# Optimization experiments

Measured on AMD Instinct MI355X. Metric: run time of the kernel, lower is better.

The kernel has to match this reference:

```python
import jax, jax.numpy as jnp
import numpy as np

B, T, D, K = 8, 4096, 512, 4096


def setup_inputs() -> dict:
    key = jax.random.key(0)
    k1, k2 = jax.random.split(key)
    x = jax.random.normal(k1, (B, T, D), dtype=jnp.float32)
    embed = jax.random.normal(k2, (K, D), dtype=jnp.float32)
    return {"x": x, "embed": embed}


def reference(x, embed):
    # F.normalize(x, p=2, dim=-1) with eps clamp like torch (eps=1e-12)
    norm = jnp.sqrt(jnp.sum(x * x, axis=-1, keepdims=True))
    xn = x / jnp.maximum(norm, 1e-12)

    flat = xn.reshape(-1, D)  # [(B*T), D]
    x_sq = jnp.sum(flat * flat, axis=1, keepdims=True)           # [(B*T), 1]
    e_sq = jnp.sum(embed * embed, axis=1)[None, :]               # [1, K]
    dist = -(x_sq - 2.0 * (flat @ embed.T) + e_sq)               # [(B*T), K]
    embed_ind = jnp.argmax(dist, axis=-1).reshape(B, T)          # [B, T]

    # decode: embedding gather then 'b n d -> b d n'
    quantize = embed[embed_ind]                                  # [B, T, D]
    quantize = jnp.transpose(quantize, (0, 2, 1))                # [B, D, T]
    return embed_ind, quantize
```

## Files before the change

### kernel.cpp

```cpp
#include <hip/hip_runtime.h>
#include <math.h>

#define BB 8
#define TT 4096
#define DDIM 512
#define KK 4096
#define NN (BB*TT)
#define EPS 0.05f

typedef __attribute__((ext_vector_type(8))) short bf16x8;
typedef __attribute__((ext_vector_type(4))) float f32x4;

__device__ __forceinline__ void async16(void* lds, const void* g) {
  __builtin_amdgcn_global_load_lds((const __attribute__((address_space(1))) void*)g,
                                   (__attribute__((address_space(3))) void*)lds, 16, 0, 0);
}

__device__ __forceinline__ unsigned pk_bf16(float a, float b) {
  unsigned ua = __float_as_uint(a); ua += 0x7FFFu + ((ua >> 16) & 1u);
  unsigned ub = __float_as_uint(b); ub += 0x7FFFu + ((ub >> 16) & 1u);
  return (ua >> 16) | (ub & 0xFFFF0000u);
}

__global__ __launch_bounds__(256) void prep_kernel(const float* __restrict__ src,
                                                   short* __restrict__ dst16,
                                                   float* __restrict__ outv, int mode) {
  int r = blockIdx.x * 4 + (threadIdx.x >> 6);
  int lane = threadIdx.x & 63;
  const float4* row4 = (const float4*)(src + (size_t)r * DDIM);
  float4 v0 = row4[lane];
  float4 v1 = row4[lane + 64];
  uint2 p0, p1;
  p0.x = pk_bf16(v0.x, v0.y); p0.y = pk_bf16(v0.z, v0.w);
  p1.x = pk_bf16(v1.x, v1.y); p1.y = pk_bf16(v1.z, v1.w);
  *(uint2*)(dst16 + (size_t)r * DDIM + lane * 4) = p0;
  *(uint2*)(dst16 + (size_t)r * DDIM + 256 + lane * 4) = p1;
  float ss = v0.x*v0.x + v0.y*v0.y + v0.z*v0.z + v0.w*v0.w
           + v1.x*v1.x + v1.y*v1.y + v1.z*v1.z + v1.w*v1.w;
  #pragma unroll
  for (int off = 32; off; off >>= 1) ss += __shfl_down(ss, off);
  if (lane == 0) outv[r] = mode ? 2.0f / fmaxf(sqrtf(ss), 1e-12f) : ss;
}

__global__ __launch_bounds__(512, 2) void vq_mfma(const short* __restrict__ xb,
                                                  const short* __restrict__ eb,
                                                  const float* __restrict__ esq,
                                                  const float* __restrict__ inv2,
                                                  float* __restrict__ out_ind,
                                                  int* __restrict__ flags,
                                                  int* __restrict__ list,
                                                  int* __restrict__ cnt) {
  __shared__ __attribute__((aligned(16))) short As[128 * 512];
  __shared__ __attribute__((aligned(16))) short Bs[2 * 256 * 32];

  const int tid = threadIdx.x;
  const int lane = tid & 63;
  const int w = tid >> 6;
  const int wr = w >> 2;
  const int wc = w & 3;
  const int q = lane >> 4, c16 = lane & 15;
  const int n0 = blockIdx.x * 128;

  #pragma unroll
  for (int j = 0; j < 16; ++j)
    async16(As + (j * 8 + w) * 512,
            xb + (size_t)(n0 + j * 8 + w) * 512 + (lane ^ w) * 8);

  const int x = (lane & 7) ^ (lane >> 3);
  const int scode = w * 16 + (lane >> 3) * 2 + (x >> 2);
  const short* gB = eb + (size_t)scode * 512 + (x & 3) * 8;
  short* sB0 = Bs + w * 512;
  async16(sB0,        gB);
  async16(sB0 + 4096, gB + 128 * 512);

  const int sigB8 = ((((c16 & 1) << 2) | q) ^ ((c16 >> 1) & 7)) * 8;
  const int brow0 = (wc * 32 + (c16 >> 1)) * 64 + sigB8;
  const int arow0 = (wr * 64 + c16) * 512;

  f32x4 iv4[4];
  #pragma unroll
  for (int ti = 0; ti < 4; ++ti)
    iv4[ti] = *(const f32x4*)&inv2[n0 + wr * 64 + ti * 16 + q * 4];

  float s1[16], s2v[16];
  int   i1[16];
  #pragma unroll
  for (int s = 0; s < 16; ++s) { s1[s] = -3e38f; s2v[s] = -3e38f; i1[s] = 0; }

  __syncthreads();

  for (int ct = 0; ct < 16; ++ct) {
    float nes[4];
    #pragma unroll
    for (int tj = 0; tj < 4; ++tj)
      nes[tj] = -esq[ct * 256 + wc * 64 + tj * 16 + c16];
    f32x4 acc[4][4];
    #pragma unroll
    for (int ti = 0; ti < 4; ++ti)
      #pragma unroll
      for (int tj = 0; tj < 4; ++tj) acc[ti][tj] = (f32x4){0.f, 0.f, 0.f, 0.f};

    #pragma unroll 2
    for (int s = 0; s < 16; ++s) {
      const int g = ct * 16 + s;
      if (g < 255) {
        const int gn = g + 1;
        const short* src = gB + (size_t)(gn >> 4) * (256 * 512) + (gn & 15) * 32;
        short* dst = Bs + ((gn & 1) << 13) + w * 512;
        async16(dst,        src);
        async16(dst + 4096, src + 128 * 512);
      }
      const short* Ap = As + arow0;
      const short* Bp = Bs + ((g & 1) << 13) + brow0;
      const int ach = ((s * 4 + q) ^ (c16 & 7)) * 8;
      bf16x8 af[4], bf[4];
      #pragma unroll
      for (int ti = 0; ti < 4; ++ti)
        af[ti] = *(const bf16x8*)(Ap + ti * 8192 + ach);
      #pragma unroll
      for (int tj = 0; tj < 4; ++tj)
        bf[tj] = *(const bf16x8*)(Bp + tj * 512);
      __builtin_amdgcn_s_setprio(1);
      #pragma unroll
      for (int ti = 0; ti < 4; ++ti)
        #pragma unroll
        for (int tj = 0; tj < 4; ++tj)
          acc[ti][tj] = __builtin_amdgcn_mfma_f32_16x16x32_bf16(af[ti], bf[tj], acc[ti][tj], 0, 0, 0);
      __builtin_amdgcn_s_setprio(0);
      __syncthreads();
    }

    const int colbase = ct * 256 + wc * 64 + c16;
    #pragma unroll
    for (int ti = 0; ti < 4; ++ti)
      #pragma unroll
      for (int r = 0; r < 4; ++r) {
        const int slot = ti * 4 + r;
        const float iv = iv4[ti][r];
        #pragma unroll
        for (int tj = 0; tj < 4; ++tj) {
          float sc = fmaf(acc[ti][tj][r], iv, nes[tj]);
          float mn = fminf(sc, s1[slot]);
          s2v[slot] = fmaxf(s2v[slot], mn);
          if (sc > s1[slot]) { s1[slot] = sc; i1[slot] = colbase + tj * 16; }
        }
      }
  }

  float* rS1 = (float*)Bs;
  float* rS2 = rS1 + 512;
  int*   rI1 = (int*)(rS2 + 512);
  #pragma unroll
  for (int slot = 0; slot < 16; ++slot) {
    float a1 = s1[slot], a2 = s2v[slot]; int ai = i1[slot];
    #pragma unroll
    for (int off = 1; off < 16; off <<= 1) {
      float b1 = __shfl_xor(a1, off);
      float b2 = __shfl_xor(a2, off);
      int   bi = __shfl_xor(ai, off);
      float mn = fminf(a1, b1);
      a2 = fmaxf(fmaxf(a2, b2), mn);
      if (b1 > a1 || (b1 == a1 && bi < ai)) { a1 = b1; ai = bi; }
    }
    if (c16 == 0) {
      int row = wr * 64 + (slot >> 2) * 16 + q * 4 + (slot & 3);
      rS1[wc * 128 + row] = a1; rS2[wc * 128 + row] = a2; rI1[wc * 128 + row] = ai;
    }
  }
  __syncthreads();
  if (tid < 128) {
    float a1 = rS1[tid], a2 = rS2[tid]; int ai = rI1[tid];
    #pragma unroll
    for (int gq = 1; gq < 4; ++gq) {
      float b1 = rS1[gq * 128 + tid], b2 = rS2[gq * 128 + tid]; int bi = rI1[gq * 128 + tid];
      float mn = fminf(a1, b1);
      a2 = fmaxf(fmaxf(a2, b2), mn);
      if (b1 > a1 || (b1 == a1 && bi < ai)) { a1 = b1; ai = bi; }
    }
    const int row = n0 + tid;
    out_ind[row] = (float)ai;
    if (a1 - a2 < EPS) {
      int p = atomicAdd(cnt, 1);
      list[p] = row;
      flags[row] = p + 1;
    } else {
      flags[row] = 0;
    }
  }
}

__global__ __launch_bounds__(256) void cleanup_kernel(const float* __restrict__ x,
                                                      const float* __restrict__ embed,
                                                      const float* __restrict__ esq,
                                                      const float* __restrict__ inv2,
                                                      const int* __restrict__ list,
                                                      const int* __restrict__ cnt,
                                                      float2* __restrict__ exact) {
  __shared__ float xr[DDIM];
  __shared__ float red_s[4];
  __shared__ int   red_i[4];
  const int rs = blockIdx.x & 31, kc = blockIdx.x >> 5;
  const int tid = threadIdx.x;
  const int lane = tid & 63, wid = tid >> 6;
  const int n = *cnt;
  for (int ii = rs; ii < n; ii += 32) {
    const int row = list[ii];
    __syncthreads();
    if (tid < 128) *(float4*)&xr[tid * 4] = *(const float4*)&x[(size_t)row * DDIM + tid * 4];
    __syncthreads();
    const float iv = inv2[row];
    float bs = -3e38f; int bi = 0;
    for (int cc = 0; cc < 2; ++cc) {
      const int code = kc * 512 + cc * 256 + tid;
      const float4* er = (const float4*)&embed[(size_t)code * DDIM];
      float acc = 0.f;
      for (int d = 0; d < DDIM / 4; ++d) {
        float4 e4 = er[d];
        float4 x4 = *(const float4*)&xr[d * 4];
        acc += x4.x * e4.x + x4.y * e4.y + x4.z * e4.z + x4.w * e4.w;
      }
      float sc = fmaf(acc, iv, -esq[code]);
      if (sc > bs || (sc == bs && code < bi)) { bs = sc; bi = code; }
    }
    #pragma unroll
    for (int off = 1; off < 64; off <<= 1) {
      float b1 = __shfl_xor(bs, off);
      int   b2 = __shfl_xor(bi, off);
      if (b1 > bs || (b1 == bs && b2 < bi)) { bs = b1; bi = b2; }
    }
    if (lane == 0) { red_s[wid] = bs; red_i[wid] = bi; }
    __syncthreads();
    if (tid == 0) {
      for (int ww = 1; ww < 4; ++ww)
        if (red_s[ww] > red_s[0] || (red_s[ww] == red_s[0] && red_i[ww] < red_i[0])) {
          red_s[0] = red_s[ww]; red_i[0] = red_i[ww];
        }
      exact[(size_t)ii * 8 + kc] = make_float2(red_s[0], (float)red_i[0]);
    }
  }
}

__global__ __launch_bounds__(256) void gather_kernel(const float* __restrict__ embed,
                                                     const int* __restrict__ flags,
                                                     const float2* __restrict__ exact,
                                                     float* __restrict__ out_ind,
                                                     float* __restrict__ out_q) {
  __shared__ int lidx[64];
  __shared__ float trans[64 * 65];
  const int n0 = blockIdx.x * 64;
  const int tid = threadIdx.x;
  if (tid < 64) {
    const int row = n0 + tid;
    const int f = flags[row];
    int idx;
    if (f) {
      float bsv = -3e38f; int bi = 0;
      const float2* e8 = &exact[(size_t)(f - 1) * 8];
      #pragma unroll
      for (int k = 0; k < 8; ++k) {
        float2 t = e8[k];
        int ci = (int)t.y;
        if (t.x > bsv || (t.x == bsv && ci < bi)) { bsv = t.x; bi = ci; }
      }
      idx = bi;
      out_ind[row] = (float)idx;
    } else {
      idx = (int)out_ind[row];
    }
    lidx[tid] = idx;
  }
  __syncthreads();
  const int bb = n0 >> 12;
  const int t0 = n0 & (TT - 1);
  const int w = tid >> 6, lane = tid & 63;
  for (int d0 = 0; d0 < DDIM; d0 += 64) {
    if (d0) __syncthreads();
    #pragma unroll
    for (int qq = 0; qq < 16; ++qq) {
      int tt2 = w * 16 + qq;
      int e = lidx[tt2];
      trans[lane * 65 + tt2] = embed[(size_t)e * DDIM + d0 + lane];
    }
    __syncthreads();
    #pragma unroll
    for (int qq = 0; qq < 4; ++qq) {
      int dl = (tid >> 4) * 4 + qq;
      int t4 = (tid & 15) * 4;
      float4 o;
      o.x = trans[dl * 65 + t4 + 0];
      o.y = trans[dl * 65 + t4 + 1];
      o.z = trans[dl * 65 + t4 + 2];
      o.w = trans[dl * 65 + t4 + 3];
      *(float4*)&out_q[((size_t)bb * DDIM + d0 + dl) * TT + t0 + t4] = o;
    }
  }
}

extern "C" void kernel_launch(void* const* d_in, const int* in_sizes, int n_in,
                              void* d_out, int out_size, void* d_ws, size_t ws_size,
                              hipStream_t stream) {
  const float* x     = (const float*)d_in[0];
  const float* embed = (const float*)d_in[1];
  char* ws = (char*)d_ws;
  short* xb      = (short*)(ws);
  short* eb      = (short*)(ws + 33554432);
  float* esq     = (float*)(ws + 37748736);
  float* inv2    = (float*)(ws + 37765120);
  int* list      = (int*)(ws + 39993344);
  int* flags     = (int*)(ws + 40124416);
  float2* exact  = (float2*)(ws + 40255488);
  int* cnt       = (int*)(ws + 42352640);

  float* out_ind = (float*)d_out;
  float* out_q   = out_ind + NN;

  prep_kernel<<<KK / 4, 256, 0, stream>>>(embed, eb, esq, 0);
  prep_kernel<<<NN / 4, 256, 0, stream>>>(x, xb, inv2, 1);
  hipMemsetAsync(cnt, 0, 4, stream);
  vq_mfma<<<256, 512, 0, stream>>>(xb, eb, esq, inv2, out_ind, flags, list, cnt);
  cleanup_kernel<<<256, 256, 0, stream>>>(x, embed, esq, inv2, list, cnt, exact);
  gather_kernel<<<NN / 64, 256, 0, stream>>>(embed, flags, exact, out_ind, out_q);
}
```

Measured before the change: 317.8 us.

## Load codebook fragments directly from global memory, dropping LDS staging and barriers

Removes the double-buffered LDS staging of the bf16 codebook tiles. Each wave now reads its B fragments straight from global memory (served by L2) into registers, so the per-k-step __syncthreads goes away, and the inner k-loop is fully unrolled. The intent is to cut barrier stalls and LDS traffic while also lowering LDS use. The cost is uncoalesced, latency-exposed global loads that have no async prefetch, and redundant reads of B across the waves in a block.

Measured after the change: 623.2 us. 1.96x slower.

```diff
diff --git a/kernel.cpp b/kernel.cpp
--- a/kernel.cpp
+++ b/kernel.cpp
@@ -51,7 +51,9 @@
                                                   int* __restrict__ list,
                                                   int* __restrict__ cnt) {
   __shared__ __attribute__((aligned(16))) short As[128 * 512];
-  __shared__ __attribute__((aligned(16))) short Bs[2 * 256 * 32];
+  __shared__ float rS1[4][128];
+  __shared__ float rS2[4][128];
+  __shared__ int   rI1[4][128];
 
   const int tid = threadIdx.x;
   const int lane = tid & 63;
@@ -66,16 +68,9 @@
     async16(As + (j * 8 + w) * 512,
             xb + (size_t)(n0 + j * 8 + w) * 512 + (lane ^ w) * 8);
 
-  const int x = (lane & 7) ^ (lane >> 3);
-  const int scode = w * 16 + (lane >> 3) * 2 + (x >> 2);
-  const short* gB = eb + (size_t)scode * 512 + (x & 3) * 8;
-  short* sB0 = Bs + w * 512;
-  async16(sB0,        gB);
-  async16(sB0 + 4096, gB + 128 * 512);
-
-  const int sigB8 = ((((c16 & 1) << 2) | q) ^ ((c16 >> 1) & 7)) * 8;
-  const int brow0 = (wc * 32 + (c16 >> 1)) * 64 + sigB8;
   const int arow0 = (wr * 64 + c16) * 512;
+
+  const short* gB = eb + (size_t)(wc * 64 + c16) * DDIM + q * 8;
 
   f32x4 iv4[4];
   #pragma unroll
@@ -90,6 +85,7 @@
   __syncthreads();
 
   for (int ct = 0; ct < 16; ++ct) {
+    const short* gBc = gB + (size_t)ct * 256 * DDIM;
     float nes[4];
     #pragma unroll
     for (int tj = 0; tj < 4; ++tj)
@@ -100,26 +96,16 @@
       #pragma unroll
       for (int tj = 0; tj < 4; ++tj) acc[ti][tj] = (f32x4){0.f, 0.f, 0.f, 0.f};
 
-    #pragma unroll 2
+    #pragma unroll
     for (int s = 0; s < 16; ++s) {
-      const int g = ct * 16 + s;
-      if (g < 255) {
-        const int gn = g + 1;
-        const short* src = gB + (size_t)(gn >> 4) * (256 * 512) + (gn & 15) * 32;
-        short* dst = Bs + ((gn & 1) << 13) + w * 512;
-        async16(dst,        src);
-        async16(dst + 4096, src + 128 * 512);
-      }
-      const short* Ap = As + arow0;
-      const short* Bp = Bs + ((g & 1) << 13) + brow0;
+      bf16x8 af[4], bf[4];
+      #pragma unroll
+      for (int tj = 0; tj < 4; ++tj)
+        bf[tj] = *(const bf16x8*)(gBc + (size_t)tj * 16 * DDIM + s * 32);
       const int ach = ((s * 4 + q) ^ (c16 & 7)) * 8;
-      bf16x8 af[4], bf[4];
       #pragma unroll
       for (int ti = 0; ti < 4; ++ti)
-        af[ti] = *(const bf16x8*)(Ap + ti * 8192 + ach);
-      #pragma unroll
-      for (int tj = 0; tj < 4; ++tj)
-        bf[tj] = *(const bf16x8*)(Bp + tj * 512);
+        af[ti] = *(const bf16x8*)(As + arow0 + ti * 8192 + ach);
       __builtin_amdgcn_s_setprio(1);
       #pragma unroll
       for (int ti = 0; ti < 4; ++ti)
@@ -127,7 +113,6 @@
         for (int tj = 0; tj < 4; ++tj)
           acc[ti][tj] = __builtin_amdgcn_mfma_f32_16x16x32_bf16(af[ti], bf[tj], acc[ti][tj], 0, 0, 0);
       __builtin_amdgcn_s_setprio(0);
-      __syncthreads();
     }
 
     const int colbase = ct * 256 + wc * 64 + c16;
@@ -147,9 +132,6 @@
       }
   }
 
-  float* rS1 = (float*)Bs;
-  float* rS2 = rS1 + 512;
-  int*   rI1 = (int*)(rS2 + 512);
   #pragma unroll
   for (int slot = 0; slot < 16; ++slot) {
     float a1 = s1[slot], a2 = s2v[slot]; int ai = i1[slot];
@@ -164,15 +146,15 @@
     }
     if (c16 == 0) {
       int row = wr * 64 + (slot >> 2) * 16 + q * 4 + (slot & 3);
-      rS1[wc * 128 + row] = a1; rS2[wc * 128 + row] = a2; rI1[wc * 128 + row] = ai;
+      rS1[wc][row] = a1; rS2[wc][row] = a2; rI1[wc][row] = ai;
     }
   }
   __syncthreads();
   if (tid < 128) {
-    float a1 = rS1[tid], a2 = rS2[tid]; int ai = rI1[tid];
+    float a1 = rS1[0][tid], a2 = rS2[0][tid]; int ai = rI1[0][tid];
     #pragma unroll
     for (int gq = 1; gq < 4; ++gq) {
-      float b1 = rS1[gq * 128 + tid], b2 = rS2[gq * 128 + tid]; int bi = rI1[gq * 128 + tid];
+      float b1 = rS1[gq][tid], b2 = rS2[gq][tid]; int bi = rI1[gq][tid];
       float mn = fminf(a1, b1);
       a2 = fmaxf(fmaxf(a2, b2), mn);
       if (b1 > a1 || (b1 == a1 && bi < ai)) { a1 = b1; ai = bi; }
```
